# Kernel optimization log

Hardware: AMD Instinct MI355X
Metric: run time of the kernel (lower is better)

Reference implementation:

```python
import jax, jax.numpy as jnp
import numpy as np

NUM_FEATURES = 81   # atom feature width used in matmuls
N_NODES = 262144
N_COLS = 103        # num_features + num_bond
OUT_CH = 128
COORD = 3           # distance rule slice [0:3]


def setup_inputs() -> dict:
    key = jax.random.key(0)
    k1, k2, k3, k4 = jax.random.split(key, 4)
    features = jax.random.normal(k1, (N_NODES, N_COLS), dtype=jnp.float32)
    # columns 81, 82 hold neighbor indices (0 => no neighbor), stored as floats
    idx = jax.random.randint(k4, (N_NODES, 2), 0, N_NODES).astype(jnp.float32)
    features = features.at[:, NUM_FEATURES:NUM_FEATURES + 2].set(idx)
    w_s = jax.random.normal(k2, (NUM_FEATURES, OUT_CH), dtype=jnp.float32) * 0.05
    w_n = jax.random.normal(k3, (N_COLS, OUT_CH), dtype=jnp.float32) * 0.05
    return {"features": features, "w_s": w_s, "w_n": w_n}


def reference(features, w_s, w_n):
    F = NUM_FEATURES
    self_f = features[:, :F]                       # [N, F]
    new_features = self_f @ w_s                    # [N, C] self term

    idx0 = features[:, F].astype(jnp.int32)        # neighbor slot 0
    idx1 = features[:, F + 1].astype(jnp.int32)    # neighbor slot 1

    def neighbor_contrib(idx):
        nei = features[idx]                                        # gather [N, 103]
        # rule 0: 'distance' over [0:COORD] -> keep neighbor slice, record distance
        d = jnp.sqrt(jnp.sum(jnp.square(self_f[:, :COORD] - nei[:, :COORD]), axis=-1))
        seg_dist = nei[:, :COORD]                                  # [N, 3]
        # rule 1: 'sum' over [COORD:F]
        seg_sum = self_f[:, COORD:F] + nei[:, COORD:F]             # [N, F-3]
        comb = jnp.concatenate([seg_dist, seg_sum], axis=-1)       # [N, F]
        d_eff = jnp.where(d > 0, d, jnp.float32(0.01))
        comb = comb / jnp.square(d_eff)[:, None]                   # distance scaling
        return comb @ w_n[:F] + new_features                       # tiny-matmul batched

    c0 = neighbor_contrib(idx0)
    c1 = neighbor_contrib(idx1)
    # rows with no valid neighbor were never written -> zeros
    out = jnp.where((idx1 != 0)[:, None], c1,
                    jnp.where((idx0 != 0)[:, None], c0, jnp.float32(0.0)))
    return out
```

## Files before the change

### kernel.cpp

```cpp
#include <hip/hip_runtime.h>
#include <hip/hip_bf16.h>

constexpr int kNodes = 262144;
constexpr int NC  = 103;
constexpr int F   = 81;
constexpr int OC  = 128;
constexpr int NKS = 6;
constexpr int NPB = 64;
constexpr int THREADS = 256;
constexpr int NST = 96;

typedef __attribute__((ext_vector_type(8))) short bf16x8;
typedef __attribute__((ext_vector_type(4))) float f32x4;
typedef float f32x4u __attribute__((ext_vector_type(4))) __attribute__((aligned(4)));

__device__ inline ushort f2bf(float f) {
  uint u = __float_as_uint(f);
  return (ushort)((u + 0x7fffu + ((u >> 16) & 1u)) >> 16);
}
__device__ inline short bfc(float x) {
  return (short)__bfloat16_as_ushort(__float2bfloat16(x));
}

__device__ __forceinline__ void gll4(const float* g, float* l) {
  __builtin_amdgcn_global_load_lds(
      (const __attribute__((address_space(1))) unsigned int*)g,
      (__attribute__((address_space(3))) unsigned int*)l, 4, 0, 0);
}

__global__ __launch_bounds__(256)
void prep_w(const float* __restrict__ w_s, const float* __restrict__ w_n,
            ushort* __restrict__ wf) {
  int t = blockIdx.x * 256 + threadIdx.x;
  if (t >= NKS * 8 * 64) return;
  int l  = t & 63;
  int ct = (t >> 6) & 7;
  int ks = t >> 9;
  int c  = ct * 16 + (l & 15);
  int kb = ks * 32 + ((l >> 4) << 3);
  union { ushort u[8]; int4 v; } o;
  #pragma unroll
  for (int i = 0; i < 8; ++i) {
    int k = kb + i;
    float f = 0.f;
    if (k < F)                      f = w_s[k * OC + c];
    else if (k >= 96 && k < 96 + F) f = w_n[(k - 96) * OC + c];
    o.u[i] = f2bf(f);
  }
  ((int4*)wf)[t] = o.v;
}

__global__ __launch_bounds__(THREADS)
void rgc_v14(const float* __restrict__ feat, const ushort* __restrict__ wf,
             float* __restrict__ out) {
  __shared__ __align__(16) float lds_nei[NPB * NST];
  __shared__ int s_sel[NPB];

  const int tid = threadIdx.x;
  const int w   = tid >> 6;
  const int l   = tid & 63;
  const long base = (long)blockIdx.x * NPB;

  const bf16x8* wfv = (const bf16x8*)wf;
  bf16x8 bA[NKS], bB[NKS];
  #pragma unroll
  for (int ks = 0; ks < NKS; ++ks) {
    bA[ks] = wfv[(ks * 8 + w)     * 64 + l];
    bB[ks] = wfv[(ks * 8 + w + 4) * 64 + l];
  }

  if (l < 16) {
    const int n = w * 16 + l;
    const float* row = feat + (base + n) * NC;
    float f0 = row[F], f1 = row[F + 1];
    int i0 = (int)f0, i1 = (int)f1;
    s_sel[n] = (i1 != 0) ? i1 : i0;
  }
  asm volatile("s_waitcnt lgkmcnt(0)" ::: "memory");
  __builtin_amdgcn_s_barrier();

  #pragma unroll
  for (int j = 0; j < 24; ++j) {
    int v   = tid + j * THREADS;
    int row = v / NST;
    int p   = v - row * NST;
    int c   = p >> 5;
    int x   = (p >> 2) & 7;
    int cl  = p & 3;
    int col = (c << 5) + ((x ^ (row & 7)) << 2) + cl;
    gll4(feat + (long)s_sel[row] * NC + col,
         lds_nei + (j * THREADS + w * 64));
  }
  asm volatile("s_waitcnt vmcnt(0)" ::: "memory");
  __builtin_amdgcn_s_barrier();

  const int q    = l >> 4;
  const int lrow = l & 15;
  const int off0 = q * 8;
  const int col  = l & 15;

  #pragma unroll 1
  for (int nt = 0; nt < 4; ++nt) {
    const int n = nt * 16 + lrow;
    const int r = n & 7;
    const float* srow = feat + (base + n) * NC;
    const float* np   = lds_nei + n * NST;
    const int sel     = s_sel[n];
    const float alive = (sel != 0) ? 1.f : 0.f;

    f32x4u s8[3][2];
    #pragma unroll
    for (int c = 0; c < 3; ++c) {
      s8[c][0] = *(const f32x4u*)(srow + c * 32 + off0);
      s8[c][1] = *(const f32x4u*)(srow + c * 32 + off0 + 4);
    }
    float sc0 = srow[0], sc1 = srow[1], sc2 = srow[2];

    float nx = np[(r << 2) + 0];
    float ny = np[(r << 2) + 1];
    float nz = np[(r << 2) + 2];
    float dx = sc0 - nx, dy = sc1 - ny, dz = sc2 - nz;
    float d2 = dx * dx + dy * dy + dz * dz;
    float cs = alive * ((d2 > 0.f) ? (1.f / d2) : 10000.f);

    bf16x8 afS[3], afC[3];
    #pragma unroll
    for (int c = 0; c < 3; ++c) {
      f32x4 lo = *(const f32x4*)(np + c * 32 + (((2 * q)     ^ r) << 2));
      f32x4 hi = *(const f32x4*)(np + c * 32 + (((2 * q + 1) ^ r) << 2));
      #pragma unroll
      for (int i = 0; i < 8; ++i) {
        float sv = s8[c][i >> 2][i & 3];
        float nv = (i < 4) ? lo[i] : hi[i - 4];
        afS[c][i] = bfc(sv * alive);
        float se = sv;
        if (c == 0 && i < 3 && q == 0) se = 0.f;
        afC[c][i] = bfc((nv + se) * cs);
      }
    }

    f32x4 a0 = (f32x4)(0.f), a1 = (f32x4)(0.f);
    #pragma unroll
    for (int ks = 0; ks < NKS; ++ks) {
      bf16x8 af = (ks < 3) ? afS[ks] : afC[ks - 3];
      a0 = __builtin_amdgcn_mfma_f32_16x16x32_bf16(af, bA[ks], a0, 0, 0, 0);
      a1 = __builtin_amdgcn_mfma_f32_16x16x32_bf16(af, bB[ks], a1, 0, 0, 0);
    }

    const long orow = base + nt * 16 + q * 4;
    #pragma unroll
    for (int rr = 0; rr < 4; ++rr) {
      out[(orow + rr) * OC + w * 16       + col] = a0[rr];
      out[(orow + rr) * OC + (w + 4) * 16 + col] = a1[rr];
    }
  }
}

extern "C" void kernel_launch(void* const* d_in, const int* in_sizes, int n_in,
                              void* d_out, int out_size, void* d_ws, size_t ws_size,
                              hipStream_t stream) {
  const float* feat = (const float*)d_in[0];
  const float* w_s  = (const float*)d_in[1];
  const float* w_n  = (const float*)d_in[2];
  float* outp = (float*)d_out;
  ushort* wf = (ushort*)d_ws;

  prep_w<<<dim3((NKS * 8 * 64 + 255) / 256), 256, 0, stream>>>(w_s, w_n, wf);
  rgc_v14<<<dim3(kNodes / NPB), THREADS, 0, stream>>>(feat, wf, outp);
}
```

Before: 78.96 us.

## Double-buffer self and neighbor tiles in LDS across multiple tiles per block

Each block now processes eight 32-node tiles instead of one 64-node tile. It stages both the contiguous self-feature rows and the gathered neighbor rows into LDS via async global-to-LDS loads, using two buffers so the next tile's loads overlap the current tile's MFMA work. Self features are read from LDS instead of unaligned global vector loads. The gain depends on hand-tuned vmcnt thresholds, and the larger LDS footprint may reduce occupancy.

```diff
diff --git a/kernel.cpp b/kernel.cpp
--- a/kernel.cpp
+++ b/kernel.cpp
@@ -6,13 +6,14 @@
 constexpr int F   = 81;
 constexpr int OC  = 128;
 constexpr int NKS = 6;
-constexpr int NPB = 64;
+constexpr int TN  = 32;
+constexpr int TPB = 8;
 constexpr int THREADS = 256;
-constexpr int NST = 96;
+constexpr int SELF_DW = 3328;
+constexpr int NEI_DW  = 3072;
 
 typedef __attribute__((ext_vector_type(8))) short bf16x8;
 typedef __attribute__((ext_vector_type(4))) float f32x4;
-typedef float f32x4u __attribute__((ext_vector_type(4))) __attribute__((aligned(4)));
 
 __device__ inline ushort f2bf(float f) {
   uint u = __float_as_uint(f);
@@ -21,8 +22,7 @@
 __device__ inline short bfc(float x) {
   return (short)__bfloat16_as_ushort(__float2bfloat16(x));
 }
-
-__device__ __forceinline__ void gll4(const float* g, float* l) {
+__device__ __forceinline__ void gll4(const float* g, const float* l) {
   __builtin_amdgcn_global_load_lds(
       (const __attribute__((address_space(1))) unsigned int*)g,
       (__attribute__((address_space(3))) unsigned int*)l, 4, 0, 0);
@@ -51,15 +51,17 @@
 }
 
 __global__ __launch_bounds__(THREADS)
-void rgc_v14(const float* __restrict__ feat, const ushort* __restrict__ wf,
+void rgc_v15(const float* __restrict__ feat, const ushort* __restrict__ wf,
              float* __restrict__ out) {
-  __shared__ __align__(16) float lds_nei[NPB * NST];
-  __shared__ int s_sel[NPB];
+  __shared__ __align__(16) float sA[2][SELF_DW];
+  __shared__ __align__(16) float sN[2][NEI_DW];
+  __shared__ int s_sel[THREADS];
 
   const int tid = threadIdx.x;
   const int w   = tid >> 6;
   const int l   = tid & 63;
-  const long base = (long)blockIdx.x * NPB;
+  const long gbase = (long)blockIdx.x * (TN * TPB);
+  const long MAXO  = (long)kNodes * NC - 1;
 
   const bf16x8* wfv = (const bf16x8*)wf;
   bf16x8 bA[NKS], bB[NKS];
@@ -69,30 +71,38 @@
     bB[ks] = wfv[(ks * 8 + w + 4) * 64 + l];
   }
 
-  if (l < 16) {
-    const int n = w * 16 + l;
-    const float* row = feat + (base + n) * NC;
+  {
+    const float* row = feat + (gbase + tid) * NC;
     float f0 = row[F], f1 = row[F + 1];
     int i0 = (int)f0, i1 = (int)f1;
-    s_sel[n] = (i1 != 0) ? i1 : i0;
+    s_sel[tid] = (i1 != 0) ? i1 : i0;
   }
   asm volatile("s_waitcnt lgkmcnt(0)" ::: "memory");
-  __builtin_amdgcn_s_barrier();
+  asm volatile("s_barrier" ::: "memory");
 
-  #pragma unroll
-  for (int j = 0; j < 24; ++j) {
-    int v   = tid + j * THREADS;
-    int row = v / NST;
-    int p   = v - row * NST;
-    int c   = p >> 5;
-    int x   = (p >> 2) & 7;
-    int cl  = p & 3;
-    int col = (c << 5) + ((x ^ (row & 7)) << 2) + cl;
-    gll4(feat + (long)s_sel[row] * NC + col,
-         lds_nei + (j * THREADS + w * 64));
+#define STAGE(T, B)                                                          \
+  {                                                                          \
+    const long tb = (gbase + (long)(T) * TN) * NC;                           \
+    _Pragma("unroll")                                                        \
+    for (int j = 0; j < 13; ++j) {            \
+      long off = tb + (j * THREADS + tid);                                   \
+      off = (off < MAXO) ? off : MAXO;                                       \
+      gll4(feat + off, &sA[B][j * THREADS + w * 64]);                        \
+    }                                                                        \
+    _Pragma("unroll")                                                        \
+    for (int j = 0; j < 12; ++j) {          \
+      int v  = tid + j * THREADS;                               \
+      int r  = v / 96;                                                       \
+      int p  = v - r * 96;                                                   \
+      int c  = p >> 5, x = (p >> 2) & 7, cl = p & 3;                         \
+      int col = (c << 5) + ((x ^ (r & 7)) << 2) + cl;                        \
+      gll4(feat + (long)s_sel[(T) * TN + r] * NC + col,                      \
+           &sN[B][j * THREADS + w * 64]);                                    \
+    }                                                                        \
   }
-  asm volatile("s_waitcnt vmcnt(0)" ::: "memory");
-  __builtin_amdgcn_s_barrier();
+
+  STAGE(0, 0);
+  STAGE(1, 1);
 
   const int q    = l >> 4;
   const int lrow = l & 15;
@@ -100,60 +110,66 @@
   const int col  = l & 15;
 
   #pragma unroll 1
-  for (int nt = 0; nt < 4; ++nt) {
-    const int n = nt * 16 + lrow;
-    const int r = n & 7;
-    const float* srow = feat + (base + n) * NC;
-    const float* np   = lds_nei + n * NST;
-    const int sel     = s_sel[n];
-    const float alive = (sel != 0) ? 1.f : 0.f;
+  for (int t = 0; t < TPB; ++t) {
+    if (t == 0)            asm volatile("s_waitcnt vmcnt(25)" ::: "memory");
+    else if (t == TPB - 1) asm volatile("s_waitcnt vmcnt(16)" ::: "memory");
+    else                   asm volatile("s_waitcnt vmcnt(41)" ::: "memory");
+    asm volatile("s_barrier" ::: "memory");
 
-    f32x4u s8[3][2];
+    const float* selfb = &sA[t & 1][0];
+    const float* neib  = &sN[t & 1][0];
+
     #pragma unroll
-    for (int c = 0; c < 3; ++c) {
-      s8[c][0] = *(const f32x4u*)(srow + c * 32 + off0);
-      s8[c][1] = *(const f32x4u*)(srow + c * 32 + off0 + 4);
-    }
-    float sc0 = srow[0], sc1 = srow[1], sc2 = srow[2];
+    for (int nt = 0; nt < 2; ++nt) {
+      const int tn = nt * 16 + lrow;
+      const int r  = tn & 7;
+      const float* sp = selfb + tn * NC;
+      const float* np = neib + tn * 96;
+      const int sel   = s_sel[t * TN + tn];
+      const float alive = (sel != 0) ? 1.f : 0.f;
 
-    float nx = np[(r << 2) + 0];
-    float ny = np[(r << 2) + 1];
-    float nz = np[(r << 2) + 2];
-    float dx = sc0 - nx, dy = sc1 - ny, dz = sc2 - nz;
-    float d2 = dx * dx + dy * dy + dz * dz;
-    float cs = alive * ((d2 > 0.f) ? (1.f / d2) : 10000.f);
+      float dx = sp[0] - np[(r << 2) + 0];
+      float dy = sp[1] - np[(r << 2) + 1];
+      float dz = sp[2] - np[(r << 2) + 2];
+      float d2 = dx * dx + dy * dy + dz * dz;
+      float cs = alive * ((d2 > 0.f) ? (1.f / d2) : 10000.f);
 
-    bf16x8 afS[3], afC[3];
-    #pragma unroll
-    for (int c = 0; c < 3; ++c) {
-      f32x4 lo = *(const f32x4*)(np + c * 32 + (((2 * q)     ^ r) << 2));
-      f32x4 hi = *(const f32x4*)(np + c * 32 + (((2 * q + 1) ^ r) << 2));
+      bf16x8 afS[3], afC[3];
       #pragma unroll
-      for (int i = 0; i < 8; ++i) {
-        float sv = s8[c][i >> 2][i & 3];
-        float nv = (i < 4) ? lo[i] : hi[i - 4];
-        afS[c][i] = bfc(sv * alive);
-        float se = sv;
-        if (c == 0 && i < 3 && q == 0) se = 0.f;
-        afC[c][i] = bfc((nv + se) * cs);
+      for (int c = 0; c < 3; ++c) {
+        f32x4 lo = *(const f32x4*)(np + c * 32 + (((2 * q)     ^ r) << 2));
+        f32x4 hi = *(const f32x4*)(np + c * 32 + (((2 * q + 1) ^ r) << 2));
+        #pragma unroll
+        for (int i = 0; i < 8; ++i) {
+          float sv = sp[c * 32 + off0 + i];
+          float nv = (i < 4) ? lo[i] : hi[i - 4];
+          afS[c][i] = bfc(sv * alive);
+          float se = sv;
+          if (c == 0 && i < 3 && q == 0) se = 0.f;
+          afC[c][i] = bfc((nv + se) * cs);
+        }
+      }
+
+      f32x4 a0 = (f32x4)(0.f), a1 = (f32x4)(0.f);
+      #pragma unroll
+      for (int ks = 0; ks < NKS; ++ks) {
+        bf16x8 af = (ks < 3) ? afS[ks] : afC[ks - 3];
+        a0 = __builtin_amdgcn_mfma_f32_16x16x32_bf16(af, bA[ks], a0, 0, 0, 0);
+        a1 = __builtin_amdgcn_mfma_f32_16x16x32_bf16(af, bB[ks], a1, 0, 0, 0);
+      }
+
+      const long orow = gbase + t * TN + nt * 16 + q * 4;
+      #pragma unroll
+      for (int rr = 0; rr < 4; ++rr) {
+        out[(orow + rr) * OC + w * 16       + col] = a0[rr];
+        out[(orow + rr) * OC + (w + 4) * 16 + col] = a1[rr];
       }
     }
 
-    f32x4 a0 = (f32x4)(0.f), a1 = (f32x4)(0.f);
-    #pragma unroll
-    for (int ks = 0; ks < NKS; ++ks) {
-      bf16x8 af = (ks < 3) ? afS[ks] : afC[ks - 3];
-      a0 = __builtin_amdgcn_mfma_f32_16x16x32_bf16(af, bA[ks], a0, 0, 0, 0);
-      a1 = __builtin_amdgcn_mfma_f32_16x16x32_bf16(af, bB[ks], a1, 0, 0, 0);
-    }
-
-    const long orow = base + nt * 16 + q * 4;
-    #pragma unroll
-    for (int rr = 0; rr < 4; ++rr) {
-      out[(orow + rr) * OC + w * 16       + col] = a0[rr];
-      out[(orow + rr) * OC + (w + 4) * 16 + col] = a1[rr];
-    }
+    asm volatile("s_barrier" ::: "memory");
+    if (t + 2 < TPB) STAGE(t + 2, t & 1);
   }
+#undef STAGE
 }
 
 extern "C" void kernel_launch(void* const* d_in, const int* in_sizes, int n_in,
@@ -166,5 +182,5 @@
   ushort* wf = (ushort*)d_ws;
 
   prep_w<<<dim3((NKS * 8 * 64 + 255) / 256), 256, 0, stream>>>(w_s, w_n, wf);
-  rgc_v14<<<dim3(kNodes / NPB), THREADS, 0, stream>>>(feat, wf, outp);
+  rgc_v15<<<dim3(kNodes / (TN * TPB)), THREADS, 0, stream>>>(feat, wf, outp);
 }
```

After: 76.32 us. 1.03x faster.
